# Optimization experiments

Hardware: AMD Instinct MI355X
Metric: run time of the kernel (lower is better)

## Reference

```python
import jax, jax.numpy as jnp
import numpy as np

GRID_SIZE = 5
GRID_RANGE = (-1.0, 1.0)


def setup_inputs() -> dict:
    key = jax.random.key(0)
    k1, k2, k3 = jax.random.split(key, 3)
    B, D, U, K = 16384, 1024, 128, GRID_SIZE + 3  # spline_order=3
    x = jax.random.normal(k1, (B, D), dtype=jnp.float32)
    # glorot-ish scale for weights
    base_weight = jax.random.normal(k2, (D, U), dtype=jnp.float32) * (1.0 / np.sqrt(D))
    spline_weight = jax.random.normal(k3, (D, U, K), dtype=jnp.float32) * (1.0 / np.sqrt(D))
    return {"x": x, "base_weight": base_weight, "spline_weight": spline_weight}


def reference(x, base_weight, spline_weight):
    # base path: SiLU(x @ W_b)
    base_out = jax.nn.silu(x @ base_weight)  # [B, U]
    # spline path: RBF over grid centers, then contract (note: x_norm in the
    # original call() is computed but unused, so it is omitted here)
    centers = jnp.linspace(GRID_RANGE[0], GRID_RANGE[1], GRID_SIZE)  # [G]
    dist = jnp.square(x[..., None] - centers)        # [B, D, G]
    rbf = jnp.exp(-5.0 * dist)                        # [B, D, G]
    spline_out = jnp.einsum('big,iug->bu', rbf, spline_weight[:, :, :GRID_SIZE])
    return base_out + spline_out
```

## Files before the change

kernel.cpp:

```cpp
#include <hip/hip_runtime.h>

typedef unsigned short u16;
typedef unsigned int u32;
typedef __bf16 bf16x8 __attribute__((ext_vector_type(8)));
typedef float f32x16 __attribute__((ext_vector_type(16)));

#define C2 (-7.213475204444817f)
#define T1C 0.28650480f
#define T2C 0.0067379470f

__device__ __forceinline__ u16 f2bf(float f) {
  u32 u = __float_as_uint(f);
  return (u16)((u + 0x7FFFu + ((u >> 16) & 1u)) >> 16);
}

__device__ __forceinline__ void async16(const void* g, void* l) {
  __builtin_amdgcn_global_load_lds(
      (const __attribute__((address_space(1))) u32*)g,
      (__attribute__((address_space(3))) u32*)l, 16, 0, 0);
}

__device__ __forceinline__ f32x16 mfma16(uint4 a, uint4 b, f32x16 c) {
  return __builtin_amdgcn_mfma_f32_32x32x16_bf16(
      __builtin_bit_cast(bf16x8, a), __builtin_bit_cast(bf16x8, b), c, 0, 0, 0);
}

__global__ __launch_bounds__(256) void kan_prep(const float* __restrict__ wb,
                                                const float* __restrict__ ws,
                                                u16* __restrict__ wst2) {
  __shared__ u16 tile[6][32][34];
  const int tid = threadIdx.x;
  const int c = blockIdx.x, ub = blockIdx.y;
#pragma unroll
  for (int it = 0; it < 4; ++it) {
    int e = it * 256 + tid;
    int dd = e >> 5, uu = e & 31;
    size_t base = (size_t)(c * 32 + dd) * 128 + ub * 32 + uu;
    const float* p = ws + base * 8;
    float4 v0 = *(const float4*)p;
    float g4 = p[4];
    tile[0][dd][uu] = f2bf(v0.x);
    tile[1][dd][uu] = f2bf(v0.y);
    tile[2][dd][uu] = f2bf(v0.z);
    tile[3][dd][uu] = f2bf(v0.w);
    tile[4][dd][uu] = f2bf(g4);
    tile[5][dd][uu] = f2bf(wb[base]);
  }
  __syncthreads();
#pragma unroll
  for (int it = 0; it < 3; ++it) {
    int idx = it * 256 + tid;
    int s = idx >> 7, r = idx & 127;
    int b8 = r >> 6, b5 = (r >> 5) & 1, l = r & 31;
    int dbase = b8 * 16 + b5 * 8;
    u32 q[4];
#pragma unroll
    for (int j = 0; j < 4; ++j) {
      u32 lo = tile[s][dbase + 2 * j][l];
      u32 hi = tile[s][dbase + 2 * j + 1][l];
      q[j] = lo | (hi << 16);
    }
    uint4 w4; w4.x = q[0]; w4.y = q[1]; w4.z = q[2]; w4.w = q[3];
    *(uint4*)(wst2 + (size_t)c * 24576 +
              (size_t)(s * 512 + b8 * 256 + ub * 64 + b5 * 32 + l) * 8) = w4;
  }
}

__global__ __launch_bounds__(512, 1) void kan_main(const float* __restrict__ x,
                                                   const u16* __restrict__ wst2,
                                                   float* __restrict__ out) {
  __shared__ __align__(16) char lds[147456];

  const int t = threadIdx.x;
  const int lane = t & 63;
  const int w = t >> 6;
  const int wm = (w >> 2) & 1, wn = (w >> 1) & 1, kks = w & 1;
  const int b0 = blockIdx.x * 64;
  const int kh = lane >> 5;

  f32x16 accs[2], accb[2];
#pragma unroll
  for (int i = 0; i < 16; ++i) {
    accs[0][i] = 0.f; accs[1][i] = 0.f;
    accb[0][i] = 0.f; accb[1][i] = 0.f;
  }

  const int wg = (w >> 2) & 1, wkk = (w >> 1) & 1, wh = w & 1;
  const u32 aw = (u32)((wg * 2 + wkk) * 1024 + wh * 512 + lane * 8);
  const float* xp = x + (size_t)(b0 + wg * 32 + (lane >> 1)) * 1024 +
                    wkk * 16 + wh * 8 + (lane & 1) * 4;

  const char* dsrcb = (const char*)wst2 + t * 16;

  const u32 ao = (u32)((wm * 2 + kks) * 1024 + lane * 16);
  const u32 bo = (u32)(24576 + (kks * 4 + wn * 2) * 1024 + lane * 16);

  auto dma = [&](int k1, char* buf) {
    const char* s0 = dsrcb + (size_t)k1 * 49152;
    char* d0 = buf + 24576 + t * 16;
#pragma unroll
    for (int s = 0; s < 6; ++s) async16(s0 + s * 8192, d0 + s * 8192);
  };

  auto rbf_write = [&](char* buf, float4 xa) {
    float xf[4] = {xa.x, xa.y, xa.z, xa.w};
    u32 rb[6][4];
#pragma unroll
    for (int e = 0; e < 4; ++e) {
      float xv = xf[e];
      float t0 = C2 * xv;
      float P = __builtin_amdgcn_exp2f(t0 * xv);
      float Qp = __builtin_amdgcn_exp2f(-t0);
      float Qm = __builtin_amdgcn_exp2f(t0);
      float PQ = P * Qp, PQm = P * Qm;
      rb[0][e] = __float_as_uint(PQm * Qm * T2C) + 0x8000u;
      rb[1][e] = __float_as_uint(PQm * T1C) + 0x8000u;
      rb[2][e] = __float_as_uint(P) + 0x8000u;
      rb[3][e] = __float_as_uint(PQ * T1C) + 0x8000u;
      rb[4][e] = __float_as_uint(PQ * Qp * T2C) + 0x8000u;
      rb[5][e] = __float_as_uint(xv) + 0x8000u;
    }
#pragma unroll
    for (int s = 0; s < 6; ++s) {
      uint2 pk;
      pk.x = __builtin_amdgcn_perm(rb[s][1], rb[s][0], 0x07060302);
      pk.y = __builtin_amdgcn_perm(rb[s][3], rb[s][2], 0x07060302);
      *(uint2*)(buf + s * 4096 + aw) = pk;
    }
  };

  float4 xreg = *(const float4*)(xp);
  dma(0, lds);
  rbf_write(lds, xreg);
  xreg = *(const float4*)(xp + 32);
  __syncthreads();

  for (int k = 0; k < 32; ++k) {
    char* cur = lds + (size_t)(k & 1) * 73728;
    if (k < 31) {
      char* nxt = lds + (size_t)((k + 1) & 1) * 73728;
      dma(k + 1, nxt);
      rbf_write(nxt, xreg);
      if (k < 30) xreg = *(const float4*)(xp + (k + 2) * 32);
    }
#pragma unroll
    for (int s = 0; s < 6; ++s) {
      uint4 a  = *(const uint4*)(cur + s * 4096 + ao);
      uint4 v0 = *(const uint4*)(cur + s * 8192 + bo);
      uint4 v1 = *(const uint4*)(cur + s * 8192 + bo + 1024);
      if (s < 5) {
        accs[0] = mfma16(a, v0, accs[0]);
        accs[1] = mfma16(a, v1, accs[1]);
      } else {
        accb[0] = mfma16(a, v0, accb[0]);
        accb[1] = mfma16(a, v1, accb[1]);
      }
    }
    __syncthreads();
  }

  const int pw = w ^ 1;
#pragma unroll
  for (int q = 0; q < 4; ++q) {
    {
      float4 s0 = make_float4(accs[0][4 * q], accs[0][4 * q + 1], accs[0][4 * q + 2], accs[0][4 * q + 3]);
      float4 s1 = make_float4(accs[1][4 * q], accs[1][4 * q + 1], accs[1][4 * q + 2], accs[1][4 * q + 3]);
      float4 b0v = make_float4(accb[0][4 * q], accb[0][4 * q + 1], accb[0][4 * q + 2], accb[0][4 * q + 3]);
      float4 b1v = make_float4(accb[1][4 * q], accb[1][4 * q + 1], accb[1][4 * q + 2], accb[1][4 * q + 3]);
      *(float4*)(lds + (w * 4 + 0) * 1024 + lane * 16) = s0;
      *(float4*)(lds + (w * 4 + 1) * 1024 + lane * 16) = s1;
      *(float4*)(lds + (w * 4 + 2) * 1024 + lane * 16) = b0v;
      *(float4*)(lds + (w * 4 + 3) * 1024 + lane * 16) = b1v;
    }
    __syncthreads();
    if (kks == 0) {
      float4 ps0 = *(const float4*)(lds + (pw * 4 + 0) * 1024 + lane * 16);
      float4 ps1 = *(const float4*)(lds + (pw * 4 + 1) * 1024 + lane * 16);
      float4 pb0 = *(const float4*)(lds + (pw * 4 + 2) * 1024 + lane * 16);
      float4 pb1 = *(const float4*)(lds + (pw * 4 + 3) * 1024 + lane * 16);
      const float* ps0f = &ps0.x; const float* ps1f = &ps1.x;
      const float* pb0f = &pb0.x; const float* pb1f = &pb1.x;
#pragma unroll
      for (int rr = 0; rr < 4; ++rr) {
        int reg = 4 * q + rr;
        int row = rr + 8 * q + 4 * kh;
        size_t m = (size_t)(b0 + wm * 32 + row);
        int n0 = wn * 64 + (lane & 31);
        float z0 = accb[0][reg] + pb0f[rr];
        float z1 = accb[1][reg] + pb1f[rr];
        float o0 = z0 / (1.0f + __expf(-z0)) + accs[0][reg] + ps0f[rr];
        float o1 = z1 / (1.0f + __expf(-z1)) + accs[1][reg] + ps1f[rr];
        out[m * 128 + n0] = o0;
        out[m * 128 + n0 + 32] = o1;
      }
    }
    __syncthreads();
  }
}

extern "C" void kernel_launch(void* const* d_in, const int* in_sizes, int n_in,
                              void* d_out, int out_size, void* d_ws, size_t ws_size,
                              hipStream_t stream) {
  const float* x  = (const float*)d_in[0];
  const float* wb = (const float*)d_in[1];
  const float* ws = (const float*)d_in[2];
  u16* wst2 = (u16*)d_ws;
  float* out = (float*)d_out;

  kan_prep<<<dim3(32, 4), 256, 0, stream>>>(wb, ws, wst2);
  kan_main<<<dim3(256), 512, 0, stream>>>(x, wst2, out);
}
```

Measured before the change: 151.8 us.

## Halve K-chunk and LDS footprint, alternate chunks between split-K wave groups

The K loop now walks 64 chunks of 16 columns instead of 32 chunks of 32, which halves the double-buffered LDS to 72KB. Launch bounds move from one block to four per SM, so more than one block can be resident if registers allow. The two split-K wave halves now take alternating chunks rather than splitting each chunk, and the weight prep kernel is rewritten to pack weights in the new 16-wide layout. The cost is twice as many barriers and smaller loads per iteration, and the 512-thread blocks with 64 accumulator registers may still fit only one or two per CU.

```diff
diff --git a/kernel.cpp b/kernel.cpp
--- a/kernel.cpp
+++ b/kernel.cpp
@@ -27,49 +27,49 @@
 
 __global__ __launch_bounds__(256) void kan_prep(const float* __restrict__ wb,
                                                 const float* __restrict__ ws,
-                                                u16* __restrict__ wst2) {
-  __shared__ u16 tile[6][32][34];
-  const int tid = threadIdx.x;
-  const int c = blockIdx.x, ub = blockIdx.y;
-#pragma unroll
-  for (int it = 0; it < 4; ++it) {
-    int e = it * 256 + tid;
-    int dd = e >> 5, uu = e & 31;
-    size_t base = (size_t)(c * 32 + dd) * 128 + ub * 32 + uu;
+                                                u16* __restrict__ wst3) {
+  __shared__ u16 tile[6][16][130];
+  const int t = threadIdx.x;
+  const int c = blockIdx.x;
+#pragma unroll
+  for (int it = 0; it < 8; ++it) {
+    int idx = it * 256 + t;
+    int d = idx >> 7, u = idx & 127;
+    size_t base = (size_t)(c * 16 + d) * 128 + u;
     const float* p = ws + base * 8;
     float4 v0 = *(const float4*)p;
     float g4 = p[4];
-    tile[0][dd][uu] = f2bf(v0.x);
-    tile[1][dd][uu] = f2bf(v0.y);
-    tile[2][dd][uu] = f2bf(v0.z);
-    tile[3][dd][uu] = f2bf(v0.w);
-    tile[4][dd][uu] = f2bf(g4);
-    tile[5][dd][uu] = f2bf(wb[base]);
+    tile[0][d][u] = f2bf(v0.x);
+    tile[1][d][u] = f2bf(v0.y);
+    tile[2][d][u] = f2bf(v0.z);
+    tile[3][d][u] = f2bf(v0.w);
+    tile[4][d][u] = f2bf(g4);
+    tile[5][d][u] = f2bf(wb[base]);
   }
   __syncthreads();
 #pragma unroll
-  for (int it = 0; it < 3; ++it) {
-    int idx = it * 256 + tid;
-    int s = idx >> 7, r = idx & 127;
-    int b8 = r >> 6, b5 = (r >> 5) & 1, l = r & 31;
-    int dbase = b8 * 16 + b5 * 8;
+  for (int i = 0; i < 6; ++i) {
+    int g = i * 256 + t;
+    int s = g >> 8, r = g & 255;
+    int nq = r >> 6, l = r & 63;
+    int u = nq * 32 + (l & 31);
+    int dbase = (l >> 5) * 8;
     u32 q[4];
 #pragma unroll
     for (int j = 0; j < 4; ++j) {
-      u32 lo = tile[s][dbase + 2 * j][l];
-      u32 hi = tile[s][dbase + 2 * j + 1][l];
+      u32 lo = tile[s][dbase + 2 * j][u];
+      u32 hi = tile[s][dbase + 2 * j + 1][u];
       q[j] = lo | (hi << 16);
     }
     uint4 w4; w4.x = q[0]; w4.y = q[1]; w4.z = q[2]; w4.w = q[3];
-    *(uint4*)(wst2 + (size_t)c * 24576 +
-              (size_t)(s * 512 + b8 * 256 + ub * 64 + b5 * 32 + l) * 8) = w4;
-  }
-}
-
-__global__ __launch_bounds__(512, 1) void kan_main(const float* __restrict__ x,
-                                                   const u16* __restrict__ wst2,
+    *(uint4*)(wst3 + (size_t)c * 12288 + (size_t)g * 8) = w4;
+  }
+}
+
+__global__ __launch_bounds__(512, 4) void kan_main(const float* __restrict__ x,
+                                                   const u16* __restrict__ wst3,
                                                    float* __restrict__ out) {
-  __shared__ __align__(16) char lds[147456];
+  __shared__ __align__(16) char lds[73728];
 
   const int t = threadIdx.x;
   const int lane = t & 63;
@@ -85,28 +85,29 @@
     accb[0][i] = 0.f; accb[1][i] = 0.f;
   }
 
-  const int wg = (w >> 2) & 1, wkk = (w >> 1) & 1, wh = w & 1;
-  const u32 aw = (u32)((wg * 2 + wkk) * 1024 + wh * 512 + lane * 8);
-  const float* xp = x + (size_t)(b0 + wg * 32 + (lane >> 1)) * 1024 +
-                    wkk * 16 + wh * 8 + (lane & 1) * 4;
-
-  const char* dsrcb = (const char*)wst2 + t * 16;
-
-  const u32 ao = (u32)((wm * 2 + kks) * 1024 + lane * 16);
-  const u32 bo = (u32)(24576 + (kks * 4 + wn * 2) * 1024 + lane * 16);
-
-  auto dma = [&](int k1, char* buf) {
-    const char* s0 = dsrcb + (size_t)k1 * 49152;
-    char* d0 = buf + 24576 + t * 16;
-#pragma unroll
-    for (int s = 0; s < 6; ++s) async16(s0 + s * 8192, d0 + s * 8192);
+  const int lp = (w & 3) * 16 + (lane >> 2);
+  const int wrow = (lp & 31) + 32 * (w >> 2);
+  const int wk = (lp >> 5) * 8 + (lane & 3) * 2;
+  const float* xp = x + (size_t)(b0 + wrow) * 1024 + wk;
+  const u32 aw = (u32)(w * 256 + lane * 4);
+
+  const char* dsrc = (const char*)wst3 + t * 16;
+
+  const u32 ao = (u32)(wm * 1024 + lane * 16);
+  const u32 bo = (u32)(12288 + wn * 2048 + lane * 16);
+
+  auto dma = [&](int c, char* buf) {
+    const char* s0 = dsrc + (size_t)c * 24576;
+    char* d0 = buf + 12288 + t * 16;
+#pragma unroll
+    for (int i = 0; i < 3; ++i) async16(s0 + i * 8192, d0 + i * 8192);
   };
 
-  auto rbf_write = [&](char* buf, float4 xa) {
-    float xf[4] = {xa.x, xa.y, xa.z, xa.w};
-    u32 rb[6][4];
-#pragma unroll
-    for (int e = 0; e < 4; ++e) {
+  auto rbf_write = [&](char* buf, float2 xa) {
+    float xf[2] = {xa.x, xa.y};
+    u32 rb[6][2];
+#pragma unroll
+    for (int e = 0; e < 2; ++e) {
       float xv = xf[e];
       float t0 = C2 * xv;
       float P = __builtin_amdgcn_exp2f(t0 * xv);
@@ -122,38 +123,38 @@
     }
 #pragma unroll
     for (int s = 0; s < 6; ++s) {
-      uint2 pk;
-      pk.x = __builtin_amdgcn_perm(rb[s][1], rb[s][0], 0x07060302);
-      pk.y = __builtin_amdgcn_perm(rb[s][3], rb[s][2], 0x07060302);
-      *(uint2*)(buf + s * 4096 + aw) = pk;
+      u32 pk = __builtin_amdgcn_perm(rb[s][1], rb[s][0], 0x07060302);
+      *(u32*)(buf + s * 2048 + aw) = pk;
     }
   };
 
-  float4 xreg = *(const float4*)(xp);
+  float2 xc = *(const float2*)(xp);
   dma(0, lds);
-  rbf_write(lds, xreg);
-  xreg = *(const float4*)(xp + 32);
+  rbf_write(lds, xc);
+  float2 xn = *(const float2*)(xp + 16);
   __syncthreads();
 
-  for (int k = 0; k < 32; ++k) {
-    char* cur = lds + (size_t)(k & 1) * 73728;
-    if (k < 31) {
-      char* nxt = lds + (size_t)((k + 1) & 1) * 73728;
-      dma(k + 1, nxt);
-      rbf_write(nxt, xreg);
-      if (k < 30) xreg = *(const float4*)(xp + (k + 2) * 32);
-    }
-#pragma unroll
-    for (int s = 0; s < 6; ++s) {
-      uint4 a  = *(const uint4*)(cur + s * 4096 + ao);
-      uint4 v0 = *(const uint4*)(cur + s * 8192 + bo);
-      uint4 v1 = *(const uint4*)(cur + s * 8192 + bo + 1024);
-      if (s < 5) {
-        accs[0] = mfma16(a, v0, accs[0]);
-        accs[1] = mfma16(a, v1, accs[1]);
-      } else {
-        accb[0] = mfma16(a, v0, accb[0]);
-        accb[1] = mfma16(a, v1, accb[1]);
+  for (int c = 0; c < 64; ++c) {
+    char* cur = lds + (size_t)(c & 1) * 36864;
+    if (c < 63) {
+      char* nxt = lds + (size_t)((c + 1) & 1) * 36864;
+      dma(c + 1, nxt);
+      rbf_write(nxt, xn);
+      if (c < 62) xn = *(const float2*)(xp + (c + 2) * 16);
+    }
+    if ((c & 1) == kks) {
+#pragma unroll
+      for (int s = 0; s < 6; ++s) {
+        uint4 a  = *(const uint4*)(cur + s * 2048 + ao);
+        uint4 v0 = *(const uint4*)(cur + s * 4096 + bo);
+        uint4 v1 = *(const uint4*)(cur + s * 4096 + bo + 1024);
+        if (s < 5) {
+          accs[0] = mfma16(a, v0, accs[0]);
+          accs[1] = mfma16(a, v1, accs[1]);
+        } else {
+          accb[0] = mfma16(a, v0, accb[0]);
+          accb[1] = mfma16(a, v1, accb[1]);
+        }
       }
     }
     __syncthreads();
@@ -204,9 +205,9 @@
   const float* x  = (const float*)d_in[0];
   const float* wb = (const float*)d_in[1];
   const float* ws = (const float*)d_in[2];
-  u16* wst2 = (u16*)d_ws;
+  u16* wst3 = (u16*)d_ws;
   float* out = (float*)d_out;
 
-  kan_prep<<<dim3(32, 4), 256, 0, stream>>>(wb, ws, wst2);
-  kan_main<<<dim3(256), 512, 0, stream>>>(x, wst2, out);
-}
+  kan_prep<<<dim3(64), 256, 0, stream>>>(wb, ws, wst3);
+  kan_main<<<dim3(256), 512, 0, stream>>>(x, wst3, out);
+}
```

Result: slower. 157.7 us (+3.9%).
